# Kernel tuning notes

Hardware: AMD Instinct MI355X
Metric: run time of the kernel (lower is better)

The kernel has to match this reference:

```python
import jax, jax.numpy as jnp
import numpy as np

N = 50000      # nodes
F = 256        # num_features
H = 128        # hidden_size
R = 16         # num_relations
E = 800000     # edges
C = 7          # num_classes
NB = 30        # num_bases (hard-coded in module)


def setup_inputs() -> dict:
    key = jax.random.key(0)
    ks = jax.random.split(key, 16)
    g = lambda k, shape, fan_in: jax.random.normal(k, shape, jnp.float32) / np.float32(np.sqrt(fan_in))
    inp = {
        "x": jax.random.normal(ks[0], (N, F), jnp.float32),
        "edge_index": jax.random.randint(ks[1], (2, E), 0, N),
        "edge_norm": jax.random.uniform(ks[2], (E,), jnp.float32),
        "edge_type": jax.random.randint(ks[3], (E,), 0, R),
        "seq_lengths": jax.random.randint(ks[4], (16,), 1, 100),
        "umask": jnp.ones((16, 110), jnp.float32),
        "nodal_attn": 0,
        "avec": 0,
        # RGCNConv (basis decomposition)
        "basis": g(ks[5], (NB, F, H), F),
        "comp": g(ks[6], (R, NB), NB),
        "root1": g(ks[7], (F, H), F),
        "bias1": jnp.zeros((H,), jnp.float32),
        # GraphConv
        "w_rel": g(ks[8], (H, H), H),
        "w_root": g(ks[9], (H, H), H),
        "bias2": jnp.zeros((H,), jnp.float32),
        # classification head
        "lin_w": g(ks[10], (F + H, H), F + H),
        "lin_b": jnp.zeros((H,), jnp.float32),
        "fc_w": g(ks[11], (H, C), H),
        "fc_b": jnp.zeros((C,), jnp.float32),
    }
    return inp


def reference(x, edge_index, edge_norm, edge_type, seq_lengths, umask,
              nodal_attn, avec, basis, comp, root1, bias1,
              w_rel, w_root, bias2, lin_w, lin_b, fc_w, fc_b):
    src, dst = edge_index[0], edge_index[1]

    # ---- RGCNConv: basis-decomposed relational conv, mean aggr per relation ----
    W = jnp.einsum('rb,bio->rio', comp, basis)          # [R,F,H]
    xW = jnp.einsum('ni,rio->nro', x, W)                # [N,R,H]
    msgs = xW[src, edge_type]                           # [E,H]
    seg = dst * R + edge_type                           # (dst, relation) segment id
    cnt = jax.ops.segment_sum(jnp.ones((E,), jnp.float32), seg, num_segments=N * R)
    inv = 1.0 / jnp.maximum(cnt, 1.0)
    agg1 = jax.ops.segment_sum(msgs * inv[seg][:, None], dst, num_segments=N)
    out1 = agg1 + x @ root1 + bias1                     # [N,H]

    # ---- GraphConv: sum aggr + root transform ----
    agg2 = jax.ops.segment_sum(out1[src], dst, num_segments=N)  # [N,H]
    out2 = agg2 @ w_rel + bias2 + out1 @ w_root         # [N,H]

    # ---- classification head (nodal_attn=False path; dropout is identity in eval) ----
    emotions = jnp.concatenate([x, out2], axis=-1)      # [N,F+H]
    hidden = jax.nn.relu(emotions @ lin_w + lin_b)      # [N,H]
    logits = hidden @ fc_w + fc_b                       # [N,C]
    return jax.nn.log_softmax(logits, axis=1)
```

## Files before the change

kernel.cpp:

```cpp
#include <hip/hip_runtime.h>
#include <hip/hip_bf16.h>
#include <stdint.h>

#define NN 50000
#define FF 256
#define HH 128
#define RR 16
#define EE 800000
#define CC 7
#define NB_ 30

typedef __attribute__((ext_vector_type(8))) short short8;
typedef __attribute__((ext_vector_type(4))) float f32x4;

__device__ __forceinline__ float bf2f(unsigned short u){
  union { unsigned int i; float f; } x; x.i = ((unsigned int)u) << 16; return x.f;
}
__device__ __forceinline__ unsigned short f2bf(float f){
  union { unsigned int i; float f; } x; x.f = f;
  unsigned int r = x.i + 0x7fffu + ((x.i >> 16) & 1u);
  return (unsigned short)(r >> 16);
}

__device__ __forceinline__ void gld16(const unsigned short* g, unsigned short* l){
  __builtin_amdgcn_global_load_lds(
      (const __attribute__((address_space(1))) unsigned int*)g,
      (__attribute__((address_space(3))) unsigned int*)l, 16, 0, 0);
}

template<bool BIAS, bool RELU, bool G1, bool FHEAD>
__global__ __launch_bounds__(256) void gemm_bt(
    const unsigned short* __restrict__ A0, int ldA0,
    const unsigned short* __restrict__ A1, int ldA1, int kSplit,
    const unsigned short* __restrict__ Bt,
    unsigned short* __restrict__ Cout, int ldC,
    const float* __restrict__ bias,
    int M, int K,
    unsigned short* __restrict__ out1, const float* __restrict__ bias1,
    const float* __restrict__ fc_w, const float* __restrict__ fc_b,
    float* __restrict__ fout)
{
  __shared__ unsigned short smem[2][128*64];
  unsigned short* Al = smem[0];
  unsigned short* Bl = smem[1];
  const int tid  = threadIdx.x;
  const int lane = tid & 63;
  const int wid  = tid >> 6;
  const int wr   = wid >> 1, wc = wid & 1;

  int bm, bn;
  if (G1){
    int orig = blockIdx.x;
    int xcd  = orig & 7, sub = orig >> 3;
    int cidx = (xcd < 7 ? xcd*831 : 7*831) + sub;
    int p    = cidx / 136;
    int wres = cidx - p*136;
    int ph   = min(8, 391 - p*8);
    bn = wres / ph;
    bm = p*8 + wres % ph;
  } else {
    bm = blockIdx.x; bn = blockIdx.y;
  }

  const int nkt = K >> 6;
  const int r8  = lane >> 3;
  const int sw  = ((lane & 7) ^ r8) * 8;

  f32x4 acc[4][4];
  #pragma unroll
  for (int m=0;m<4;m++)
    #pragma unroll
    for (int n=0;n<4;n++) acc[m][n] = (f32x4){0.f,0.f,0.f,0.f};

  for (int kt=0; kt<nkt; ++kt){
    int c0 = kt*64;
    const unsigned short* Asrc = A0; int lda = ldA0;
    if (c0 >= kSplit){ Asrc = A1; lda = ldA1; c0 -= kSplit; }
    const unsigned short* arow = Asrc + (size_t)(bm*128 + wid*32 + r8)*lda + c0 + sw;
    const unsigned short* brow = Bt   + (size_t)(bn*128 + wid*32 + r8)*K  + kt*64 + sw;
    #pragma unroll
    for (int i=0;i<4;i++){
      gld16(arow + (size_t)(i*8)*lda, &Al[(wid*32 + i*8)*64]);
      gld16(brow + (size_t)(i*8)*K,   &Bl[(wid*32 + i*8)*64]);
    }
    __syncthreads();
    #pragma unroll
    for (int ks=0; ks<2; ++ks){
      const int slot = ((ks<<2) + (lane>>4)) ^ (lane&7);
      short8 a[4], b[4];
      #pragma unroll
      for (int m=0;m<4;m++)
        a[m] = *(const short8*)&Al[(wr*64 + m*16 + (lane&15))*64 + slot*8];
      #pragma unroll
      for (int n=0;n<4;n++)
        b[n] = *(const short8*)&Bl[(wc*64 + n*16 + (lane&15))*64 + slot*8];
      #pragma unroll
      for (int m=0;m<4;m++)
        #pragma unroll
        for (int n=0;n<4;n++)
          acc[m][n] = __builtin_amdgcn_mfma_f32_16x16x32_bf16(b[n], a[m], acc[m][n], 0, 0, 0);
    }
    __syncthreads();
  }

  if (FHEAD){
    unsigned int* Hu = (unsigned int*)smem;
    #pragma unroll
    for (int m=0;m<4;m++){
      int row = wr*64 + m*16 + (lane&15);
      #pragma unroll
      for (int n=0;n<4;n++){
        int cbase = wc*64 + n*16 + ((lane>>4)<<2);
        float v0 = acc[m][n][0] + bias[cbase];
        float v1 = acc[m][n][1] + bias[cbase+1];
        float v2 = acc[m][n][2] + bias[cbase+2];
        float v3 = acc[m][n][3] + bias[cbase+3];
        v0 = fmaxf(v0,0.f); v1 = fmaxf(v1,0.f); v2 = fmaxf(v2,0.f); v3 = fmaxf(v3,0.f);
        int cp = (cbase>>1) ^ ((row&7)<<1);
        Hu[row*64 + cp    ] = (unsigned int)f2bf(v0) | ((unsigned int)f2bf(v1) << 16);
        Hu[row*64 + cp + 1] = (unsigned int)f2bf(v2) | ((unsigned int)f2bf(v3) << 16);
      }
    }
    __syncthreads();
    float w0[CC], w1[CC];
    #pragma unroll
    for (int c=0;c<CC;c++){
      w0[c] = fc_w[(lane*2)*CC + c];
      w1[c] = fc_w[(lane*2+1)*CC + c];
    }
    for (int i=0;i<32;i++){
      int r = wid*32 + i;
      int node = bm*128 + r;
      if (node >= NN) break;
      unsigned int h = Hu[r*64 + (((lane>>1) ^ (r&7))<<1) + (lane&1)];
      float h0 = bf2f((unsigned short)h);
      float h1 = bf2f((unsigned short)(h>>16));
      float lg[CC];
      #pragma unroll
      for (int c=0;c<CC;c++){
        float p = h0*w0[c] + h1*w1[c];
        #pragma unroll
        for (int off=32; off; off>>=1) p += __shfl_down(p, off, 64);
        lg[c] = p;
      }
      if (lane == 0){
        float l[CC]; float mx = -1e30f;
        #pragma unroll
        for (int c=0;c<CC;c++){ l[c] = lg[c] + fc_b[c]; mx = fmaxf(mx, l[c]); }
        float s = 0.f;
        #pragma unroll
        for (int c=0;c<CC;c++) s += expf(l[c]-mx);
        float lse = logf(s);
        #pragma unroll
        for (int c=0;c<CC;c++) fout[(size_t)node*CC + c] = l[c] - mx - lse;
      }
    }
    return;
  }

  #pragma unroll
  for (int m=0;m<4;m++){
    int row = bm*128 + wr*64 + m*16 + (lane&15);
    if (row < M){
      #pragma unroll
      for (int n=0;n<4;n++){
        int colr = wc*64 + n*16 + ((lane>>4)<<2);
        float v0 = acc[m][n][0], v1 = acc[m][n][1], v2 = acc[m][n][2], v3 = acc[m][n][3];
        if (G1){
          if (bn == 16){
            v0 += bias1[colr]; v1 += bias1[colr+1]; v2 += bias1[colr+2]; v3 += bias1[colr+3];
            unsigned int lo = (unsigned int)f2bf(v0) | ((unsigned int)f2bf(v1) << 16);
            unsigned int hi = (unsigned int)f2bf(v2) | ((unsigned int)f2bf(v3) << 16);
            *(uint2*)&out1[(size_t)row*HH + colr] = make_uint2(lo, hi);
          } else {
            unsigned int lo = (unsigned int)f2bf(v0) | ((unsigned int)f2bf(v1) << 16);
            unsigned int hi = (unsigned int)f2bf(v2) | ((unsigned int)f2bf(v3) << 16);
            *(uint2*)&Cout[(size_t)row*2048 + bn*128 + colr] = make_uint2(lo, hi);
          }
        } else {
          int col = bn*128 + colr;
          if (BIAS){ v0 += bias[col]; v1 += bias[col+1]; v2 += bias[col+2]; v3 += bias[col+3]; }
          if (RELU){ v0 = fmaxf(v0,0.f); v1 = fmaxf(v1,0.f); v2 = fmaxf(v2,0.f); v3 = fmaxf(v3,0.f); }
          unsigned int lo = (unsigned int)f2bf(v0) | ((unsigned int)f2bf(v1) << 16);
          unsigned int hi = (unsigned int)f2bf(v2) | ((unsigned int)f2bf(v3) << 16);
          *(uint2*)&Cout[(size_t)row*ldC + col] = make_uint2(lo, hi);
        }
      }
    }
  }
}

__global__ void k_cvt(const float* __restrict__ in, unsigned short* __restrict__ out, int n4){
  int i = blockIdx.x*256 + threadIdx.x;
  if (i >= n4) return;
  float4 v = ((const float4*)in)[i];
  union { unsigned short u[4]; uint2 q; } t;
  t.u[0]=f2bf(v.x); t.u[1]=f2bf(v.y); t.u[2]=f2bf(v.z); t.u[3]=f2bf(v.w);
  ((uint2*)out)[i] = t.q;
}

__global__ __launch_bounds__(256) void k_build_wt(const float* __restrict__ comp,
                                                  const float* __restrict__ basis,
                                                  unsigned short* __restrict__ WT){
  __shared__ float sm[16][129];
  __shared__ float cmp[NB_];
  int r = blockIdx.x >> 4, i0 = (blockIdx.x & 15)*16;
  int o = threadIdx.x & 127, ih = threadIdx.x >> 7;
  if (threadIdx.x < NB_) cmp[threadIdx.x] = comp[r*NB_ + threadIdx.x];
  __syncthreads();
  #pragma unroll
  for (int step=0; step<8; ++step){
    int i = i0 + step*2 + ih;
    float s = 0.f;
    #pragma unroll 6
    for (int b=0;b<NB_;b++) s += cmp[b]*basis[((size_t)b*FF + i)*HH + o];
    sm[step*2+ih][o] = s;
  }
  __syncthreads();
  #pragma unroll
  for (int w=0;w<8;w++){
    int o2 = w*16 + (threadIdx.x>>4);
    int ii = threadIdx.x & 15;
    WT[((size_t)(r*128 + o2))*FF + i0 + ii] = f2bf(sm[ii][o2]);
  }
}

__global__ void k_transpose_cat(const float* __restrict__ in0, int k0,
                                const float* __restrict__ in1, int k1,
                                unsigned short* __restrict__ outT){
  int K = k0 + k1;
  int idx = blockIdx.x*256 + threadIdx.x;
  if (idx >= 128*K) return;
  int o = idx / K, k = idx % K;
  float v = (k < k0) ? in0[(size_t)k*HH + o] : in1[(size_t)(k-k0)*HH + o];
  outT[idx] = f2bf(v);
}

__global__ void k_count(const int* __restrict__ dstv, int* __restrict__ counts){
  int e = blockIdx.x*256 + threadIdx.x;
  if (e >= EE) return;
  atomicAdd(&counts[dstv[e]], 1);
}

__global__ __launch_bounds__(256) void k_scan1(const int* __restrict__ counts,
                                               int* __restrict__ row_ptr,
                                               int* __restrict__ blocksum){
  __shared__ int wsum[4];
  int g = blockIdx.x*256 + threadIdx.x;
  int lane = threadIdx.x & 63, wv = threadIdx.x >> 6;
  int v = (g < NN) ? counts[g] : 0;
  int s = v;
  #pragma unroll
  for (int off=1; off<64; off<<=1){ int t = __shfl_up(s, off, 64); if (lane>=off) s += t; }
  if (lane==63) wsum[wv] = s;
  __syncthreads();
  int wo = 0;
  #pragma unroll
  for (int i=0;i<4;i++) if (i < wv) wo += wsum[i];
  int incl = s + wo;
  if (g < NN) row_ptr[g] = incl - v;
  if (threadIdx.x == 255) blocksum[blockIdx.x] = incl;
}
__global__ __launch_bounds__(256) void k_scan2(int* __restrict__ blocksum, int nb){
  __shared__ int wsum[4];
  int t = threadIdx.x, lane = t & 63, wv = t >> 6;
  int v = (t < nb) ? blocksum[t] : 0;
  int s = v;
  #pragma unroll
  for (int off=1; off<64; off<<=1){ int u = __shfl_up(s, off, 64); if (lane>=off) s += u; }
  if (lane==63) wsum[wv] = s;
  __syncthreads();
  int wo = 0;
  #pragma unroll
  for (int i=0;i<4;i++) if (i < wv) wo += wsum[i];
  if (t < nb) blocksum[t] = s + wo - v;
}
__global__ __launch_bounds__(256) void k_scan3(int* __restrict__ row_ptr,
                                               const int* __restrict__ blocksum){
  int g = blockIdx.x*256 + threadIdx.x;
  if (g < NN) row_ptr[g] += blocksum[blockIdx.x];
  if (g == 0) row_ptr[NN] = EE;
}

__global__ void k_fill(const int* __restrict__ srcv, const int* __restrict__ dstv,
                       const int* __restrict__ etv, const int* __restrict__ row_ptr,
                       int* __restrict__ cursor, int* __restrict__ packed){
  int e = blockIdx.x*256 + threadIdx.x;
  if (e >= EE) return;
  int d = dstv[e];
  int p = atomicAdd(&cursor[d], 1);
  packed[row_ptr[d] + p] = (srcv[e] & 0xffff) | (etv[e] << 16);
}

__global__ __launch_bounds__(256) void k_agg1(const int* __restrict__ row_ptr,
                                              const int* __restrict__ packed,
                                              const unsigned int* __restrict__ xWu,
                                              unsigned int* __restrict__ out1u){
  __shared__ int   cnt[4][RR];
  __shared__ float inv[4][RR];
  const int lane = threadIdx.x & 63;
  const int wv   = threadIdx.x >> 6;
  const int node = blockIdx.x*4 + wv;
  if (lane < RR) cnt[wv][lane] = 0;
  __syncthreads();
  const int b0 = row_ptr[node], b1 = row_ptr[node+1];
  for (int j=b0+lane; j<b1; j+=64) atomicAdd(&cnt[wv][(packed[j]>>16)&15], 1);
  __syncthreads();
  if (lane < RR) inv[wv][lane] = 1.0f / fmaxf((float)cnt[wv][lane], 1.0f);
  __syncthreads();

  float a0=0.f, a1=0.f;
  int j = b0;
  for (; j+8 <= b1; j+=8){
    int pv[8]; unsigned int vv[8];
    #pragma unroll
    for (int q=0;q<8;q++) pv[q] = packed[j+q];
    #pragma unroll
    for (int q=0;q<8;q++)
      vv[q] = xWu[((size_t)(((pv[q]&0xffff)<<4)|((pv[q]>>16)&15)) << 6) + lane];
    #pragma unroll
    for (int q=0;q<8;q++){
      float f = inv[wv][(pv[q]>>16)&15];
      a0 += bf2f((unsigned short)vv[q])*f;
      a1 += bf2f((unsigned short)(vv[q]>>16))*f;
    }
  }
  for (; j+4 <= b1; j+=4){
    int pv[4]; unsigned int vv[4];
    #pragma unroll
    for (int q=0;q<4;q++) pv[q] = packed[j+q];
    #pragma unroll
    for (int q=0;q<4;q++)
      vv[q] = xWu[((size_t)(((pv[q]&0xffff)<<4)|((pv[q]>>16)&15)) << 6) + lane];
    #pragma unroll
    for (int q=0;q<4;q++){
      float f = inv[wv][(pv[q]>>16)&15];
      a0 += bf2f((unsigned short)vv[q])*f;
      a1 += bf2f((unsigned short)(vv[q]>>16))*f;
    }
  }
  for (; j<b1; ++j){
    int p = packed[j];
    unsigned int v = xWu[((size_t)(((p&0xffff)<<4)|((p>>16)&15)) << 6) + lane];
    float f = inv[wv][(p>>16)&15];
    a0 += bf2f((unsigned short)v)*f;
    a1 += bf2f((unsigned short)(v>>16))*f;
  }
  size_t o = (size_t)node*64 + lane;
  unsigned int cur = out1u[o];
  float r0 = bf2f((unsigned short)cur)       + a0;
  float r1 = bf2f((unsigned short)(cur>>16)) + a1;
  out1u[o] = (unsigned int)f2bf(r0) | ((unsigned int)f2bf(r1) << 16);
}

__global__ __launch_bounds__(256) void k_agg2(const int* __restrict__ row_ptr,
                                              const int* __restrict__ packed,
                                              const unsigned int* __restrict__ out1u,
                                              unsigned int* __restrict__ agg2u){
  const int lane = threadIdx.x & 63;
  const int wv   = threadIdx.x >> 6;
  const int node = blockIdx.x*4 + wv;
  const int b0 = row_ptr[node], b1 = row_ptr[node+1];
  float a0=0.f, a1=0.f;
  int j = b0;
  for (; j+8 <= b1; j+=8){
    unsigned int vv[8];
    #pragma unroll
    for (int q=0;q<8;q++)
      vv[q] = out1u[(size_t)(packed[j+q]&0xffff)*64 + lane];
    #pragma unroll
    for (int q=0;q<8;q++){
      a0 += bf2f((unsigned short)vv[q]);
      a1 += bf2f((unsigned short)(vv[q]>>16));
    }
  }
  for (; j+4 <= b1; j+=4){
    unsigned int vv[4];
    #pragma unroll
    for (int q=0;q<4;q++)
      vv[q] = out1u[(size_t)(packed[j+q]&0xffff)*64 + lane];
    #pragma unroll
    for (int q=0;q<4;q++){
      a0 += bf2f((unsigned short)vv[q]);
      a1 += bf2f((unsigned short)(vv[q]>>16));
    }
  }
  for (; j<b1; ++j){
    unsigned int v = out1u[(size_t)(packed[j]&0xffff)*64 + lane];
    a0 += bf2f((unsigned short)v);
    a1 += bf2f((unsigned short)(v>>16));
  }
  agg2u[(size_t)node*64 + lane] = (unsigned int)f2bf(a0) | ((unsigned int)f2bf(a1) << 16);
}

extern "C" void kernel_launch(void* const* d_in, const int* in_sizes, int n_in,
                              void* d_out, int out_size, void* d_ws, size_t ws_size,
                              hipStream_t stream)
{
  const float* x      = (const float*)d_in[0];
  const int*   eidx   = (const int*)d_in[1];
  const int*   etype  = (const int*)d_in[3];
  const float* basis  = (const float*)d_in[8];
  const float* comp   = (const float*)d_in[9];
  const float* root1  = (const float*)d_in[10];
  const float* bias1  = (const float*)d_in[11];
  const float* w_rel  = (const float*)d_in[12];
  const float* w_root = (const float*)d_in[13];
  const float* bias2  = (const float*)d_in[14];
  const float* lin_w  = (const float*)d_in[15];
  const float* lin_b  = (const float*)d_in[16];
  const float* fc_w   = (const float*)d_in[17];
  const float* fc_b   = (const float*)d_in[18];
  const int* srcv = eidx;
  const int* dstv = eidx + EE;

  char* w = (char*)d_ws;
  unsigned short* x_bf    = (unsigned short*)(w + 0);
  unsigned short* xW      = (unsigned short*)(w + 25624576);
  unsigned short* out2_bf = (unsigned short*)(w + 25624576 + 12812288);
  unsigned short* agg2_bf = (unsigned short*)(w + 25624576 + 25624576);
  unsigned short* WT      = (unsigned short*)(w + 230424576);
  unsigned short* rootT   = (unsigned short*)(w + 231473152);
  unsigned short* W2T     = (unsigned short*)(w + 231538688);
  unsigned short* linT    = (unsigned short*)(w + 231604224);
  unsigned short* out1_bf = (unsigned short*)(w + 231702528);
  int*            counts  = (int*)(w + 244514816);
  int*            row_ptr = (int*)(w + 244715008);
  int*            cursor  = (int*)(w + 244915200);
  int*            packed  = (int*)(w + 245115392);
  int*            blocksum= (int*)(w + 248315392);
  (void)rootT;

  hipMemsetAsync(counts, 0, NN*4, stream);
  hipMemsetAsync(cursor, 0, NN*4, stream);

  k_cvt<<<12500, 256, 0, stream>>>(x, x_bf, NN*FF/4);
  k_build_wt<<<256, 256, 0, stream>>>(comp, basis, WT);
  k_transpose_cat<<<128, 256, 0, stream>>>(root1, 256, nullptr, 0, rootT);
  k_transpose_cat<<<128, 256, 0, stream>>>(w_rel, 128, w_root, 128, W2T);
  k_transpose_cat<<<192, 256, 0, stream>>>(lin_w, 384, nullptr, 0, linT);

  k_count<<<3125, 256, 0, stream>>>(dstv, counts);
  k_scan1<<<196, 256, 0, stream>>>(counts, row_ptr, blocksum);
  k_scan2<<<1, 256, 0, stream>>>(blocksum, 196);
  k_scan3<<<196, 256, 0, stream>>>(row_ptr, blocksum);
  k_fill<<<3125, 256, 0, stream>>>(srcv, dstv, etype, row_ptr, cursor, packed);

  gemm_bt<false,false,true,false><<<6647, 256, 0, stream>>>(
      x_bf, FF, nullptr, 0, 1<<30, WT, xW, 2048, nullptr, NN, FF,
      out1_bf, bias1, nullptr, nullptr, nullptr);
  k_agg1<<<12500, 256, 0, stream>>>(row_ptr, packed, (const unsigned int*)xW, (unsigned int*)out1_bf);
  k_agg2<<<12500, 256, 0, stream>>>(row_ptr, packed, (const unsigned int*)out1_bf, (unsigned int*)agg2_bf);
  {
    dim3 g(391, 1);
    gemm_bt<true,false,false,false><<<g, 256, 0, stream>>>(
        agg2_bf, HH, out1_bf, HH, HH, W2T, out2_bf, HH, bias2, NN, 2*HH,
        nullptr, nullptr, nullptr, nullptr, nullptr);
  }
  {
    dim3 g(391, 1);
    gemm_bt<true,true,false,true><<<g, 256, 0, stream>>>(
        x_bf, FF, out2_bf, HH, FF, linT, nullptr, HH, lin_b, NN, FF+HH,
        nullptr, nullptr, fc_w, fc_b, (float*)d_out);
  }
}
```

Before: 440.7 us.

## Load GEMM operands directly from global into registers, dropping LDS staging

Replaces the LDS-staged tile loads (global_load_lds plus barriers) in the bf16 MFMA GEMM with direct per-lane 16-byte global loads of A and B fragments into registers. This removes the two __syncthreads per k-tile and the LDS footprint in the non-head variants, which may raise occupancy. In exchange, each wave fetches its own operands and the 2x2 wave layout loads every A and B fragment twice, so the kernel relies on L1/L2 hits and loses LDS-based sharing across waves.

```diff
diff --git a/kernel.cpp b/kernel.cpp
--- a/kernel.cpp
+++ b/kernel.cpp
@@ -20,12 +20,6 @@
   union { unsigned int i; float f; } x; x.f = f;
   unsigned int r = x.i + 0x7fffu + ((x.i >> 16) & 1u);
   return (unsigned short)(r >> 16);
-}
-
-__device__ __forceinline__ void gld16(const unsigned short* g, unsigned short* l){
-  __builtin_amdgcn_global_load_lds(
-      (const __attribute__((address_space(1))) unsigned int*)g,
-      (__attribute__((address_space(3))) unsigned int*)l, 16, 0, 0);
 }
 
 template<bool BIAS, bool RELU, bool G1, bool FHEAD>
@@ -40,9 +34,7 @@
     const float* __restrict__ fc_w, const float* __restrict__ fc_b,
     float* __restrict__ fout)
 {
-  __shared__ unsigned short smem[2][128*64];
-  unsigned short* Al = smem[0];
-  unsigned short* Bl = smem[1];
+  __shared__ unsigned int Hu[FHEAD ? 128*64 : 4];
   const int tid  = threadIdx.x;
   const int lane = tid & 63;
   const int wid  = tid >> 6;
@@ -62,52 +54,43 @@
     bm = blockIdx.x; bn = blockIdx.y;
   }
 
-  const int nkt = K >> 6;
-  const int r8  = lane >> 3;
-  const int sw  = ((lane & 7) ^ r8) * 8;
+  const int nkt  = K >> 6;
+  const int rsel = lane & 15;
+  const int kg   = (lane >> 4) * 8;
 
   f32x4 acc[4][4];
   #pragma unroll
   for (int m=0;m<4;m++)
     #pragma unroll
     for (int n=0;n<4;n++) acc[m][n] = (f32x4){0.f,0.f,0.f,0.f};
+
+  const unsigned short* bb0 = Bt + (size_t)(bn*128 + wc*64 + rsel)*K + kg;
 
   for (int kt=0; kt<nkt; ++kt){
     int c0 = kt*64;
     const unsigned short* Asrc = A0; int lda = ldA0;
     if (c0 >= kSplit){ Asrc = A1; lda = ldA1; c0 -= kSplit; }
-    const unsigned short* arow = Asrc + (size_t)(bm*128 + wid*32 + r8)*lda + c0 + sw;
-    const unsigned short* brow = Bt   + (size_t)(bn*128 + wid*32 + r8)*K  + kt*64 + sw;
-    #pragma unroll
-    for (int i=0;i<4;i++){
-      gld16(arow + (size_t)(i*8)*lda, &Al[(wid*32 + i*8)*64]);
-      gld16(brow + (size_t)(i*8)*K,   &Bl[(wid*32 + i*8)*64]);
-    }
-    __syncthreads();
+    const unsigned short* ab = Asrc + (size_t)(bm*128 + wr*64 + rsel)*lda + c0 + kg;
+    const unsigned short* bb = bb0 + kt*64;
     #pragma unroll
     for (int ks=0; ks<2; ++ks){
-      const int slot = ((ks<<2) + (lane>>4)) ^ (lane&7);
       short8 a[4], b[4];
       #pragma unroll
-      for (int m=0;m<4;m++)
-        a[m] = *(const short8*)&Al[(wr*64 + m*16 + (lane&15))*64 + slot*8];
-      #pragma unroll
-      for (int n=0;n<4;n++)
-        b[n] = *(const short8*)&Bl[(wc*64 + n*16 + (lane&15))*64 + slot*8];
+      for (int m=0;m<4;m++) a[m] = *(const short8*)(ab + (size_t)(m*16)*lda + ks*32);
+      #pragma unroll
+      for (int n=0;n<4;n++) b[n] = *(const short8*)(bb + (size_t)(n*16)*K + ks*32);
       #pragma unroll
       for (int m=0;m<4;m++)
         #pragma unroll
         for (int n=0;n<4;n++)
           acc[m][n] = __builtin_amdgcn_mfma_f32_16x16x32_bf16(b[n], a[m], acc[m][n], 0, 0, 0);
     }
-    __syncthreads();
   }
 
   if (FHEAD){
-    unsigned int* Hu = (unsigned int*)smem;
     #pragma unroll
     for (int m=0;m<4;m++){
-      int row = wr*64 + m*16 + (lane&15);
+      int row = wr*64 + m*16 + rsel;
       #pragma unroll
       for (int n=0;n<4;n++){
         int cbase = wc*64 + n*16 + ((lane>>4)<<2);
@@ -160,7 +143,7 @@
 
   #pragma unroll
   for (int m=0;m<4;m++){
-    int row = bm*128 + wr*64 + m*16 + (lane&15);
+    int row = bm*128 + wr*64 + m*16 + rsel;
     if (row < M){
       #pragma unroll
       for (int n=0;n<4;n++){
```

Result: slower. 562.8 us (+27.7%).
